# Kernel tuning notes

Measured on AMD Instinct MI355X. Metric: run time of the kernel, lower is better.

The kernel has to match this reference:

```python
import jax, jax.numpy as jnp
import numpy as np

B, H, K, HID = 64, 32, 4096, 7168
Q_LORA, KV_LORA = 1536, 512
NOPE, ROPE, VDIM = 128, 64, 128
HEAD_SIZE = NOPE + ROPE  # 192
EPS = 1e-6
SOFTMAX_SCALE = HEAD_SIZE ** -0.5  # mscale = 1 (no yarn)


def rmsnorm(x, w, eps=EPS):
    return x * jax.lax.rsqrt(jnp.mean(x * x, axis=-1, keepdims=True) + eps) * w


def interleave_rope(x, cos, sin):
    # x: [..., ROPE]; replicate torch view(d//2,2).transpose(2,3).reshape(d):
    # interleaved [r0,i0,r1,i1,...] -> [r0,r1,...,i0,i1,...], then rotate-half RoPE.
    shp = x.shape
    x = jnp.swapaxes(x.reshape(shp[:-1] + (ROPE // 2, 2)), -1, -2).reshape(shp)
    x1, x2 = x[..., : ROPE // 2], x[..., ROPE // 2:]
    # cos/sin: [B, ROPE//2] -> broadcast over head axis
    c = cos[:, None, :]
    s = sin[:, None, :]
    return jnp.concatenate([x1 * c - x2 * s, x2 * c + x1 * s], axis=-1)


def setup_inputs() -> dict:
    key = jax.random.key(0)
    ks = jax.random.split(key, 12)
    w = 0.02
    return {
        "hidden_states": jax.random.normal(ks[0], (B, HID), jnp.float32),
        "cos": jax.random.uniform(ks[1], (B, ROPE // 2), jnp.float32),
        "sin": jax.random.uniform(ks[2], (B, ROPE // 2), jnp.float32),
        "kv_cache": jax.random.normal(ks[3], (B, K, KV_LORA + ROPE), jnp.float32),
        "w_q_a": jax.random.normal(ks[4], (HID, Q_LORA), jnp.float32) * w,
        "q_a_ln_w": jnp.ones((Q_LORA,), jnp.float32),
        "w_q_b": jax.random.normal(ks[5], (Q_LORA, H * HEAD_SIZE), jnp.float32) * w,
        "w_kv_a": jax.random.normal(ks[6], (HID, KV_LORA + ROPE), jnp.float32) * w,
        "kv_a_ln_w": jnp.ones((KV_LORA,), jnp.float32),
        "w_uk_t": jax.random.normal(ks[7], (H, NOPE, KV_LORA), jnp.float32) * w,
        "w_uv": jax.random.normal(ks[8], (H, KV_LORA, VDIM), jnp.float32) * w,
        "w_o": jax.random.normal(ks[9], (H * VDIM, HID), jnp.float32) * w,
        "slots": jnp.full((B,), K - 1, jnp.int32),
        "seq_lens": jnp.full((B,), K, jnp.int32),
    }


def reference(hidden_states, cos, sin, kv_cache, w_q_a, q_a_ln_w, w_q_b,
              w_kv_a, kv_a_ln_w, w_uk_t, w_uv, w_o, slots, seq_lens):
    # --- Q low-rank path: q_a_proj -> RMSNorm -> q_b_proj ---
    q_c = rmsnorm(hidden_states @ w_q_a, q_a_ln_w)          # [B, Q_LORA]
    q = (q_c @ w_q_b).reshape(B, H, HEAD_SIZE)              # [B, H, 192]
    q_nope, q_pe = q[..., :NOPE], q[..., NOPE:]

    # --- K-up absorption: ql_nope = q_nope @ W_UK_T (per head) ---
    ql_nope = jnp.einsum("bhn,hnr->bhr", q_nope, w_uk_t)    # [B, H, KV_LORA]

    # --- compressed KV projection ---
    ckv = hidden_states @ w_kv_a                            # [B, KV_LORA+ROPE]
    kv_c, k_pe = ckv[:, :KV_LORA], ckv[:, KV_LORA:]
    kv_c = rmsnorm(kv_c, kv_a_ln_w)                         # [B, KV_LORA]
    k_pe = k_pe[:, None, :]                                 # [B, 1, ROPE]

    # --- interleaved RoPE on pe parts ---
    q_pe = interleave_rope(q_pe, cos, sin)                  # [B, H, ROPE]
    k_pe = interleave_rope(k_pe, cos, sin)[:, 0, :]         # [B, ROPE]

    # --- latent cache writeback ---
    latent_k = jnp.concatenate([kv_c, k_pe], axis=-1)       # [B, KV_LORA+ROPE]
    cache = kv_cache.at[jnp.arange(B), slots].set(latent_k)  # [B, K, 576]

    # --- MLA latent attention (decode) ---
    query = jnp.concatenate([ql_nope, q_pe], axis=-1)       # [B, H, 576]
    scores = jnp.einsum("bhd,bkd->bhk", query, cache) * SOFTMAX_SCALE
    valid = (jnp.arange(K)[None, :] < seq_lens[:, None])[:, None, :]  # [B,1,K]
    scores = jnp.where(valid, scores, jnp.finfo(scores.dtype).min)
    probs = jax.nn.softmax(scores, axis=-1)                 # [B, H, K]
    attn = jnp.einsum("bhk,bkr->bhr", probs, cache[..., :KV_LORA])  # [B,H,KV_LORA]

    # --- V-up absorption + output projection ---
    out = jnp.einsum("bhr,hrv->bhv", attn, w_uv)            # [B, H, VDIM]
    return out.reshape(B, H * VDIM) @ w_o                   # [B, HID]
```

## Files before the change

### kernel.cpp

```cpp
#include <hip/hip_runtime.h>
#include <stdint.h>

#define NB 64
#define NH 32
#define KCTX 4096
#define HID 7168
#define QLORA 1536
#define KVL 512
#define DTOT 576
#define NSPLIT 4
#define KSPAN 1024
#define NTILE 64
#define TK 16
#define SM_SCALE 0.07216878364870323f
#define NEGINF (-3.0e38f)

typedef __attribute__((ext_vector_type(4))) float f32x4;
typedef __attribute__((ext_vector_type(8))) __bf16 bf16x8;

#define LGKM_BARRIER() do{ asm volatile("s_waitcnt lgkmcnt(0)" ::: "memory"); __builtin_amdgcn_s_barrier(); } while(0)

static __device__ __forceinline__ void glds16(const void* g, void* s){
    __builtin_amdgcn_global_load_lds((const __attribute__((address_space(1))) void*)g,
                                     (__attribute__((address_space(3))) void*)s, 16, 0, 0);
}

static __device__ __forceinline__ unsigned short f2bf(float f){
    union{__bf16 h; unsigned short s;} x; x.h = (__bf16)f; return x.s;
}
static __device__ __forceinline__ float bf2f(unsigned short h){
    union{unsigned i;float f;}x; x.i=((unsigned)h)<<16; return x.f;
}
static __device__ __forceinline__ unsigned pack2(float a, float b){
    union{__bf16 h[2]; unsigned u;} x; x.h[0]=(__bf16)a; x.h[1]=(__bf16)b; return x.u;
}

template<int OUT_MODE>
static __device__ __forceinline__ void gemm_core_packed(
        const unsigned short* __restrict__ Ahi, const unsigned short* __restrict__ Alo,
        const float* __restrict__ Wm, float* __restrict__ P, int N, int ksteps,
        int bx, int by,
        unsigned short* Ah, unsigned short* Al, unsigned short* Bh, unsigned short* Bl)
{
    const int tid = threadIdx.x;
    const int w = tid>>6, l = tid&63, lm = l&15, lg = l>>4;
    const int n0 = bx*64;
    const int s  = by;
    const int mn = tid&63, ks = tid>>6;
    const int widx = ((mn>>4)*64 + ks*16 + (mn&15));

    f32x4 acc[4];
#pragma unroll
    for (int i=0;i<4;++i){ acc[i][0]=0.f; acc[i][1]=0.f; acc[i][2]=0.f; acc[i][3]=0.f; }

    uint4 ah4, al4; float wv[8];
    auto load_raw = [&](int t){
        const int k0 = (s*ksteps + t)*32;
        size_t gidx = (size_t)((k0>>3) + ks)*64 + mn;
        ah4 = *(const uint4*)(Ahi + gidx*8);
        al4 = *(const uint4*)(Alo + gidx*8);
        const float* wp = Wm + (size_t)(k0 + ks*8)*N + n0 + mn;
#pragma unroll
        for (int j=0;j<8;++j) wv[j] = wp[(size_t)j*N];
    };
    auto cvt_write = [&](int buf){
        unsigned short h8[8], l8[8];
#pragma unroll
        for (int j=0;j<8;++j){
            h8[j] = f2bf(wv[j]);
            l8[j] = f2bf(wv[j] - bf2f(h8[j]));
        }
        uint4 bh4, bl4;
        bh4.x=(unsigned)h8[0]|((unsigned)h8[1]<<16); bh4.y=(unsigned)h8[2]|((unsigned)h8[3]<<16);
        bh4.z=(unsigned)h8[4]|((unsigned)h8[5]<<16); bh4.w=(unsigned)h8[6]|((unsigned)h8[7]<<16);
        bl4.x=(unsigned)l8[0]|((unsigned)l8[1]<<16); bl4.y=(unsigned)l8[2]|((unsigned)l8[3]<<16);
        bl4.z=(unsigned)l8[4]|((unsigned)l8[5]<<16); bl4.w=(unsigned)l8[6]|((unsigned)l8[7]<<16);
        *(uint4*)(Ah + buf*2048 + widx*8) = ah4;
        *(uint4*)(Al + buf*2048 + widx*8) = al4;
        *(uint4*)(Bh + buf*2048 + widx*8) = bh4;
        *(uint4*)(Bl + buf*2048 + widx*8) = bl4;
    };

    load_raw(0);
    for (int t=0; t<ksteps; ++t){
        const int buf = t&1;
        cvt_write(buf);
        __syncthreads();
        if (t+1 < ksteps) load_raw(t+1);
        const int fa = buf*2048 + (w*64 + lg*16 + lm)*8;
        bf16x8 fah = *(const bf16x8*)(Ah + fa);
        bf16x8 fal = *(const bf16x8*)(Al + fa);
#pragma unroll
        for (int nt=0;nt<4;++nt){
            const int fb = buf*2048 + (nt*64 + lg*16 + lm)*8;
            bf16x8 fbh = *(const bf16x8*)(Bh + fb);
            bf16x8 fbl = *(const bf16x8*)(Bl + fb);
            acc[nt] = __builtin_amdgcn_mfma_f32_16x16x32_bf16(fah, fbh, acc[nt], 0,0,0);
            acc[nt] = __builtin_amdgcn_mfma_f32_16x16x32_bf16(fal, fbh, acc[nt], 0,0,0);
            acc[nt] = __builtin_amdgcn_mfma_f32_16x16x32_bf16(fah, fbl, acc[nt], 0,0,0);
        }
        __syncthreads();
    }
#pragma unroll
    for (int nt=0;nt<4;++nt){
        int n = n0 + nt*16 + lm;
#pragma unroll
        for (int r=0;r<4;++r){
            int m = w*16 + lg*4 + r;
            if (OUT_MODE == 0) P[((size_t)s*64 + m)*N + n] = acc[nt][r];
            else               unsafeAtomicAdd(&P[(size_t)m*N + n], acc[nt][r]);
        }
    }
}

static __device__ __forceinline__ void gemm_core_raw(
        const float* __restrict__ Araw, int KA,
        const float* __restrict__ Wm, float* __restrict__ P, int N, int ksteps,
        int bx, int by,
        unsigned short* Ah, unsigned short* Al, unsigned short* Bh, unsigned short* Bl)
{
    const int tid = threadIdx.x;
    const int w = tid>>6, l = tid&63, lm = l&15, lg = l>>4;
    const int n0 = bx*64;
    const int s  = by;
    const int mn = tid&63, ks = tid>>6;
    const int widx = ((mn>>4)*64 + ks*16 + (mn&15));

    f32x4 acc[4];
#pragma unroll
    for (int i=0;i<4;++i){ acc[i][0]=0.f; acc[i][1]=0.f; acc[i][2]=0.f; acc[i][3]=0.f; }

    float av[8], wv[8];
    auto load_raw = [&](int t){
        const int k0 = (s*ksteps + t)*32;
        const float* ap = Araw + (size_t)mn*KA + k0 + ks*8;
        *(float4*)(av)   = *(const float4*)(ap);
        *(float4*)(av+4) = *(const float4*)(ap+4);
        const float* wp = Wm + (size_t)(k0 + ks*8)*N + n0 + mn;
#pragma unroll
        for (int j=0;j<8;++j) wv[j] = wp[(size_t)j*N];
    };
    auto cvt_write = [&](int buf){
        unsigned short ha[8], la[8], hb[8], lb[8];
#pragma unroll
        for (int j=0;j<8;++j){
            ha[j] = f2bf(av[j]); la[j] = f2bf(av[j] - bf2f(ha[j]));
            hb[j] = f2bf(wv[j]); lb[j] = f2bf(wv[j] - bf2f(hb[j]));
        }
        uint4 ah4, al4, bh4, bl4;
        ah4.x=(unsigned)ha[0]|((unsigned)ha[1]<<16); ah4.y=(unsigned)ha[2]|((unsigned)ha[3]<<16);
        ah4.z=(unsigned)ha[4]|((unsigned)ha[5]<<16); ah4.w=(unsigned)ha[6]|((unsigned)ha[7]<<16);
        al4.x=(unsigned)la[0]|((unsigned)la[1]<<16); al4.y=(unsigned)la[2]|((unsigned)la[3]<<16);
        al4.z=(unsigned)la[4]|((unsigned)la[5]<<16); al4.w=(unsigned)la[6]|((unsigned)la[7]<<16);
        bh4.x=(unsigned)hb[0]|((unsigned)hb[1]<<16); bh4.y=(unsigned)hb[2]|((unsigned)hb[3]<<16);
        bh4.z=(unsigned)hb[4]|((unsigned)hb[5]<<16); bh4.w=(unsigned)hb[6]|((unsigned)hb[7]<<16);
        bl4.x=(unsigned)lb[0]|((unsigned)lb[1]<<16); bl4.y=(unsigned)lb[2]|((unsigned)lb[3]<<16);
        bl4.z=(unsigned)lb[4]|((unsigned)lb[5]<<16); bl4.w=(unsigned)lb[6]|((unsigned)lb[7]<<16);
        *(uint4*)(Ah + buf*2048 + widx*8) = ah4;
        *(uint4*)(Al + buf*2048 + widx*8) = al4;
        *(uint4*)(Bh + buf*2048 + widx*8) = bh4;
        *(uint4*)(Bl + buf*2048 + widx*8) = bl4;
    };

    load_raw(0);
    for (int t=0; t<ksteps; ++t){
        const int buf = t&1;
        cvt_write(buf);
        __syncthreads();
        if (t+1 < ksteps) load_raw(t+1);
        const int fa = buf*2048 + (w*64 + lg*16 + lm)*8;
        bf16x8 fah = *(const bf16x8*)(Ah + fa);
        bf16x8 fal = *(const bf16x8*)(Al + fa);
#pragma unroll
        for (int nt=0;nt<4;++nt){
            const int fb = buf*2048 + (nt*64 + lg*16 + lm)*8;
            bf16x8 fbh = *(const bf16x8*)(Bh + fb);
            bf16x8 fbl = *(const bf16x8*)(Bl + fb);
            acc[nt] = __builtin_amdgcn_mfma_f32_16x16x32_bf16(fah, fbh, acc[nt], 0,0,0);
            acc[nt] = __builtin_amdgcn_mfma_f32_16x16x32_bf16(fal, fbh, acc[nt], 0,0,0);
            acc[nt] = __builtin_amdgcn_mfma_f32_16x16x32_bf16(fah, fbl, acc[nt], 0,0,0);
        }
        __syncthreads();
    }
#pragma unroll
    for (int nt=0;nt<4;++nt){
        int n = n0 + nt*16 + lm;
#pragma unroll
        for (int r=0;r<4;++r){
            int m = w*16 + lg*4 + r;
            P[((size_t)s*64 + m)*N + n] = acc[nt][r];
        }
    }
}

__global__ __launch_bounds__(256) void gemm_mfma(
        const unsigned short* __restrict__ Ahi, const unsigned short* __restrict__ Alo,
        const float* __restrict__ Wm, float* __restrict__ P, int N, int ksteps)
{
    __shared__ unsigned short Ah[2*2048], Al[2*2048], Bh[2*2048], Bl[2*2048];
    gemm_core_packed<0>(Ahi, Alo, Wm, P, N, ksteps, blockIdx.x, blockIdx.y, Ah, Al, Bh, Bl);
}

__global__ __launch_bounds__(256) void gemm_atomic(
        const unsigned short* __restrict__ Ahi, const unsigned short* __restrict__ Alo,
        const float* __restrict__ Wm, float* __restrict__ Out, int N, int ksteps)
{
    __shared__ unsigned short Ah[2*2048], Al[2*2048], Bh[2*2048], Bl[2*2048];
    gemm_core_packed<1>(Ahi, Alo, Wm, Out, N, ksteps, blockIdx.x, blockIdx.y, Ah, Al, Bh, Bl);
}

__global__ __launch_bounds__(256) void gemm_dual_raw(
        const float* __restrict__ Araw, int KA,
        const float* __restrict__ W0, float* __restrict__ P0, int N0, int ks0, int nbx0, int nblk0,
        const float* __restrict__ W1, float* __restrict__ P1, int N1, int ks1, int nbx1)
{
    __shared__ unsigned short Ah[2*2048], Al[2*2048], Bh[2*2048], Bl[2*2048];
    int bid = blockIdx.x;
    if (bid < nblk0){
        gemm_core_raw(Araw, KA, W0, P0, N0, ks0, bid%nbx0, bid/nbx0, Ah, Al, Bh, Bl);
    } else {
        bid -= nblk0;
        gemm_core_raw(Araw, KA, W1, P1, N1, ks1, bid%nbx1, bid/nbx1, Ah, Al, Bh, Bl);
    }
}

static __device__ __forceinline__ void rms_core(const float* __restrict__ P,
        const float* __restrict__ w, unsigned short* __restrict__ Hi,
        unsigned short* __restrict__ Lo, int S, int b, float* red)
{
    const int t = threadIdx.x;
    float v[6]; float ss = 0.f;
#pragma unroll
    for (int j=0;j<6;++j){
        int n = j*256 + t;
        float s = 0.f;
        for (int sp=0; sp<S; ++sp) s += P[((size_t)sp*64+b)*1536 + n];
        v[j] = s; ss += s*s;
    }
#pragma unroll
    for (int off=32; off>=1; off>>=1) ss += __shfl_xor(ss, off, 64);
    if ((t&63)==0) red[t>>6] = ss;
    __syncthreads();
    float tot = red[0]+red[1]+red[2]+red[3];
    float rs = rsqrtf(tot/1536.f + 1e-6f);
#pragma unroll
    for (int j=0;j<6;++j){
        int n = j*256+t;
        float val = v[j]*rs*w[n];
        unsigned short hs = f2bf(val);
        unsigned short ls = f2bf(val - bf2f(hs));
        size_t ui = (size_t)(n>>3)*512 + b*8 + (n&7);
        Hi[ui] = hs; Lo[ui] = ls;
    }
}

static __device__ __forceinline__ void kvrope_core(const float* __restrict__ P,
        const float* __restrict__ w, const float* __restrict__ cosb, const float* __restrict__ sinb,
        float* __restrict__ latent, int S, int b, float* vals, float* red)
{
    const int t = threadIdx.x;
    float ss = 0.f;
    for (int j=0;j<3;++j){
        int n = j*256+t;
        if (n < 576){
            float s=0.f;
            for (int sp=0;sp<S;++sp) s += P[((size_t)sp*64+b)*576 + n];
            vals[n]=s;
            if (n<512) ss += s*s;
        }
    }
#pragma unroll
    for (int off=32; off>=1; off>>=1) ss += __shfl_xor(ss, off, 64);
    if ((t&63)==0) red[t>>6]=ss;
    __syncthreads();
    float tot = red[0]+red[1]+red[2]+red[3];
    float rs = rsqrtf(tot/512.f + 1e-6f);
    for (int j=0;j<3;++j){
        int n = j*256+t;
        if (n<576){
            float o;
            if (n < 512) o = vals[n]*rs*w[n];
            else if (n < 544){ int i=n-512; o = vals[512+2*i]*cosb[b*32+i] - vals[513+2*i]*sinb[b*32+i]; }
            else            { int i=n-544; o = vals[513+2*i]*cosb[b*32+i] + vals[512+2*i]*sinb[b*32+i]; }
            latent[(size_t)b*576 + n] = o;
        }
    }
}

__global__ __launch_bounds__(256) void norm_dual(
        const float* __restrict__ Pq, const float* __restrict__ qw,
        unsigned short* __restrict__ Hi, unsigned short* __restrict__ Lo, int Sq,
        const float* __restrict__ Pkv, const float* __restrict__ kvw,
        const float* __restrict__ cosb, const float* __restrict__ sinb,
        float* __restrict__ latent, int Skv)
{
    __shared__ float vals[576];
    __shared__ float red[4];
    if (blockIdx.x < 64) rms_core(Pq, qw, Hi, Lo, Sq, blockIdx.x, red);
    else                 kvrope_core(Pkv, kvw, cosb, sinb, latent, Skv, blockIdx.x-64, vals, red);
}

__global__ __launch_bounds__(256) void finish_q(const float* __restrict__ P,
        const float* __restrict__ cosb, const float* __restrict__ sinb,
        unsigned short* __restrict__ qh, unsigned short* __restrict__ ql,
        float* __restrict__ query, int S)
{
    int i = blockIdx.x*256 + threadIdx.x;
    int b = i / 6144, n = i - b*6144;
    float s = 0.f;
    for (int sp=0; sp<S; ++sp) s += P[((size_t)sp*64+b)*6144 + n];
    int h = n/192, nl = n - h*192;
    if (nl < 128){
        unsigned short hs = f2bf(s);
        unsigned short ls = f2bf(s - bf2f(hs));
        size_t ui = (size_t)h*8192 + (size_t)(nl>>3)*512 + b*8 + (nl&7);
        qh[ui]=hs; ql[ui]=ls;
    } else {
        int i2 = (nl-128)>>1;
        float other = __shfl_xor(s, 1);
        float c = cosb[b*32+i2], sn = sinb[b*32+i2];
        float* o = query + ((size_t)b*32+h)*576;
        if ((nl&1)==0) o[512+i2] = s*c - other*sn;
        else           o[544+i2] = s*c + other*sn;
    }
}

__global__ __launch_bounds__(256) void qlnope_mfma(const unsigned short* __restrict__ qh,
        const unsigned short* __restrict__ ql,
        const float* __restrict__ wukt, float* __restrict__ query)
{
    __shared__ unsigned short Bh[4096], Bl[4096];
    const int h = blockIdx.x, r0 = blockIdx.y*128;
    const int tid = threadIdx.x;
    const int w = tid>>6, l = tid&63, lm = l&15, lg = l>>4;
    f32x4 acc[8];
#pragma unroll
    for (int i=0;i<8;++i){ acc[i][0]=0.f; acc[i][1]=0.f; acc[i][2]=0.f; acc[i][3]=0.f; }

    for (int ck=0; ck<4; ++ck){
        const int k0 = ck*32;
        unsigned short hh[2][8], ll[2][8]; int wid0 = tid*2;
#pragma unroll
        for (int wi=0; wi<2; ++wi){
            int wid = wid0 + wi;
            int ntile = wid>>6, kg = (wid>>4)&3, nl = wid&15;
            int n = r0 + ntile*16 + nl;
            const float* wp = wukt + (size_t)h*65536 + (size_t)(k0+kg*8)*512 + n;
#pragma unroll
            for (int j=0;j<8;++j){
                float v = wp[(size_t)j*512];
                hh[wi][j] = f2bf(v);
                ll[wi][j] = f2bf(v - bf2f(hh[wi][j]));
            }
        }
        __syncthreads();
#pragma unroll
        for (int wi=0; wi<2; ++wi){
            int wid = wid0 + wi;
            uint4 uh, ul;
            uh.x=(unsigned)hh[wi][0]|((unsigned)hh[wi][1]<<16); uh.y=(unsigned)hh[wi][2]|((unsigned)hh[wi][3]<<16);
            uh.z=(unsigned)hh[wi][4]|((unsigned)hh[wi][5]<<16); uh.w=(unsigned)hh[wi][6]|((unsigned)hh[wi][7]<<16);
            ul.x=(unsigned)ll[wi][0]|((unsigned)ll[wi][1]<<16); ul.y=(unsigned)ll[wi][2]|((unsigned)ll[wi][3]<<16);
            ul.z=(unsigned)ll[wi][4]|((unsigned)ll[wi][5]<<16); ul.w=(unsigned)ll[wi][6]|((unsigned)ll[wi][7]<<16);
            *(uint4*)(Bh + wid*8) = uh;
            *(uint4*)(Bl + wid*8) = ul;
        }
        __syncthreads();
        size_t ai = (size_t)h*8192 + (size_t)(ck*4+lg)*512 + (size_t)(w*16+lm)*8;
        union{uint4 u; bf16x8 v;} fh, fl;
        fh.u = *(const uint4*)(qh + ai);
        fl.u = *(const uint4*)(ql + ai);
#pragma unroll
        for (int nt=0;nt<8;++nt){
            const int fb = (nt*64 + lg*16 + lm)*8;
            bf16x8 fbh = *(const bf16x8*)(Bh + fb);
            bf16x8 fbl = *(const bf16x8*)(Bl + fb);
            acc[nt] = __builtin_amdgcn_mfma_f32_16x16x32_bf16(fh.v, fbh, acc[nt], 0,0,0);
            acc[nt] = __builtin_amdgcn_mfma_f32_16x16x32_bf16(fl.v, fbh, acc[nt], 0,0,0);
            acc[nt] = __builtin_amdgcn_mfma_f32_16x16x32_bf16(fh.v, fbl, acc[nt], 0,0,0);
        }
        __syncthreads();
    }
#pragma unroll
    for (int nt=0;nt<8;++nt){
        int r = r0 + nt*16 + lm;
#pragma unroll
        for (int qq=0;qq<4;++qq){
            int bb = w*16 + lg*4 + qq;
            query[((size_t)bb*32 + h)*576 + r] = acc[nt][qq];
        }
    }
}

static __device__ __forceinline__ int vt_addr(int d, int key){
    return (d>>2)*64 + (((d&3)^((d>>3)&3))<<4) + key;
}

__global__ __launch_bounds__(512,1) void attn_mfma(const float* __restrict__ query,
        const float* __restrict__ kv, const float* __restrict__ latent,
        const int* __restrict__ slots, const int* __restrict__ seq_lens,
        float* __restrict__ Opart, float* __restrict__ Mpart, float* __restrict__ Lpart)
{
    __shared__ float Kf[3][16*576];
    __shared__ unsigned short Vt[8192];
    __shared__ float S_s[8][32][16];
    __shared__ unsigned short P_s[32][40];
    __shared__ float alpha_s[32];

    const int b = blockIdx.y, sp = blockIdx.x;
    const int tid = threadIdx.x;
    const int w = tid>>6, l = tid&63;
    const int lm = l&15, lg = l>>4;
    const int ht = w&1;
    const int dg = w>>1;
    const int cs = 2*w + (w>=1?1:0) + (w>=5?1:0);
    const int cnt = ((w&3)==0)?3:2;
    const int seqlen = seq_lens[b];
    const int slot = slots[b];
    const int k0 = sp*KSPAN;
    const int myh = tid>>4, s5 = tid&15;

    P_s[tid>>4][16 + (tid&15)] = 0;

    bf16x8 qf[2][3];
#pragma unroll
    for (int h2=0; h2<2; ++h2){
        const float* qrow = query + ((size_t)b*32 + h2*16 + lm)*576;
#pragma unroll
        for (int ss=0;ss<3;++ss){
            union{uint4 u; bf16x8 v;} cv;
            if (ss < cnt){
                int d0 = (cs+ss)*32 + lg*8;
                float4 a = *(const float4*)(qrow + d0);
                float4 c = *(const float4*)(qrow + d0 + 4);
                cv.u.x=pack2(a.x,a.y); cv.u.y=pack2(a.z,a.w);
                cv.u.z=pack2(c.x,c.y); cv.u.w=pack2(c.z,c.w);
            } else {
                cv.u.x=0; cv.u.y=0; cv.u.z=0; cv.u.w=0;
            }
            qf[h2][ss]=cv.v;
        }
    }

    auto issue_tile = [&](int tt, int buf){
        const int gkb = k0 + tt*TK;
#pragma unroll
        for (int i=0;i<5;++i){
            int s = i*8 + w;
            if (s < 36){
                int B = s*1024 + l*16;
                int r = B / 2304;
                int gs = (B - r*2304) >> 4;
                int g  = gs ^ (r&7);
                int gk = gkb + r; if (gk > KCTX-1) gk = KCTX-1;
                const float* src = (gk==slot) ? (latent + (size_t)b*576 + g*4)
                                              : (kv + ((size_t)b*KCTX + gk)*576 + g*4);
                glds16(src, ((char*)&Kf[buf][0]) + B);
            }
        }
    };

    f32x4 oacc[8];
#pragma unroll
    for (int i=0;i<8;++i){ oacc[i][0]=0.f; oacc[i][1]=0.f; oacc[i][2]=0.f; oacc[i][3]=0.f; }
    float m_run = NEGINF, l_run = 0.f;

    issue_tile(0, 0);
    issue_tile(1, 1);
    if (w < 4) { asm volatile("s_waitcnt vmcnt(5)" ::: "memory"); }
    else       { asm volatile("s_waitcnt vmcnt(4)" ::: "memory"); }
    __builtin_amdgcn_s_barrier();

    int cur = 0;
    for (int tt=0; tt<NTILE; ++tt){
        if (tt+2 < NTILE){
            int ib = cur+2; if (ib>=3) ib-=3;
            issue_tile(tt+2, ib);
        }

        {
            const int kg = tid&1;
            const int dq = (tid>>1)&127;
            const int rep = tid>>8;
            float4 rv[4];
#pragma unroll
            for (int i=0;i<4;++i){
                int r = kg*8 + rep*4 + i;
                rv[i] = *(const float4*)(&Kf[cur][r*576 + ((dq ^ (r&7))<<2)]);
            }
#pragma unroll
            for (int j=0;j<4;++j){
                uint2 o;
                o.x = pack2(((const float*)&rv[0])[j], ((const float*)&rv[1])[j]);
                o.y = pack2(((const float*)&rv[2])[j], ((const float*)&rv[3])[j]);
                *(uint2*)(Vt + vt_addr(dq*4+j, kg*8) + rep*4) = o;
            }
        }
        {
            f32x4 s0, s1;
            s0[0]=0.f; s0[1]=0.f; s0[2]=0.f; s0[3]=0.f;
            s1[0]=0.f; s1[1]=0.f; s1[2]=0.f; s1[3]=0.f;
            const float* kb = &Kf[cur][lm*576];
            const int sw = lm&7;
            __builtin_amdgcn_s_setprio(1);
#pragma unroll
            for (int ss=0;ss<3;++ss){
                if (ss < cnt){
                    int g = (cs+ss)*8 + lg*2;
                    float4 fa = *(const float4*)(kb + ((g ^ sw)<<2));
                    float4 fb = *(const float4*)(kb + (((g+1) ^ sw)<<2));
                    union{uint4 u; bf16x8 v;} cv;
                    cv.u.x = pack2(fa.x, fa.y); cv.u.y = pack2(fa.z, fa.w);
                    cv.u.z = pack2(fb.x, fb.y); cv.u.w = pack2(fb.z, fb.w);
                    s0 = __builtin_amdgcn_mfma_f32_16x16x32_bf16(qf[0][ss], cv.v, s0, 0,0,0);
                    s1 = __builtin_amdgcn_mfma_f32_16x16x32_bf16(qf[1][ss], cv.v, s1, 0,0,0);
                }
            }
            __builtin_amdgcn_s_setprio(0);
#pragma unroll
            for (int r=0;r<4;++r){
                S_s[w][(lg<<2)+r][lm]      = s0[r];
                S_s[w][16+(lg<<2)+r][lm]   = s1[r];
            }
        }
        LGKM_BARRIER();

        {
            const int kbase = k0 + tt*TK;
            float v = 0.f;
#pragma unroll
            for (int i=0;i<8;++i) v += S_s[i][myh][s5];
            v *= SM_SCALE;
            float sc = (kbase + s5 < seqlen) ? v : NEGINF;
            float tmax = sc;
            tmax = fmaxf(tmax, __shfl_xor(tmax,1));
            tmax = fmaxf(tmax, __shfl_xor(tmax,2));
            tmax = fmaxf(tmax, __shfl_xor(tmax,4));
            tmax = fmaxf(tmax, __shfl_xor(tmax,8));
            float mnew = fmaxf(m_run, tmax);
            float al = __expf(m_run - mnew);
            float pv = (sc > 0.5f*NEGINF) ? __expf(sc-mnew) : 0.f;
            P_s[myh][s5] = f2bf(pv);
            float ps = pv;
            ps += __shfl_xor(ps,1); ps += __shfl_xor(ps,2);
            ps += __shfl_xor(ps,4); ps += __shfl_xor(ps,8);
            l_run = l_run*al + ps;
            m_run = mnew;
            if (s5==0) alpha_s[myh] = al;
        }
        LGKM_BARRIER();

        {
            float al4[4];
#pragma unroll
            for (int r=0;r<4;++r) al4[r] = alpha_s[ht*16 + (lg<<2) + r];
            bf16x8 pa = *(const bf16x8*)(&P_s[ht*16+lm][lg*8]);
            __builtin_amdgcn_s_setprio(1);
#pragma unroll
            for (int nt=0;nt<8;++nt){
                f32x4 o = oacc[nt];
                o[0]*=al4[0]; o[1]*=al4[1]; o[2]*=al4[2]; o[3]*=al4[3];
                int r = dg*128 + nt*16 + lm;
                bf16x8 bv = *(const bf16x8*)(Vt + vt_addr(r, (lg&1)*8));
                oacc[nt] = __builtin_amdgcn_mfma_f32_16x16x32_bf16(pa, bv, o, 0,0,0);
            }
            __builtin_amdgcn_s_setprio(0);
        }
        if (tt+2 < NTILE){
            if (w < 4) { asm volatile("s_waitcnt vmcnt(5)" ::: "memory"); }
            else       { asm volatile("s_waitcnt vmcnt(4)" ::: "memory"); }
            __builtin_amdgcn_s_barrier();
        } else if (tt+1 < NTILE){
            asm volatile("s_waitcnt vmcnt(0)" ::: "memory");
            __builtin_amdgcn_s_barrier();
        }
        cur = cur+1; if (cur>=3) cur-=3;
    }

    const int obase = (b*NSPLIT+sp)*32;
#pragma unroll
    for (int nt=0;nt<8;++nt){
        int r = dg*128 + nt*16 + lm;
#pragma unroll
        for (int qq=0;qq<4;++qq){
            int h = ht*16 + (lg<<2) + qq;
            Opart[((size_t)(obase+h))*512 + r] = oacc[nt][qq];
        }
    }
    if (s5==0){ Mpart[obase+myh]=m_run; Lpart[obase+myh]=l_run; }
}

__global__ __launch_bounds__(256) void av_uv_merge(const float* __restrict__ Opart,
        const float* __restrict__ Mpart, const float* __restrict__ Lpart,
        const float* __restrict__ wuv,
        unsigned short* __restrict__ Hi, unsigned short* __restrict__ Lo)
{
    __shared__ unsigned short Bh[4096], Bl[4096];
    __shared__ unsigned short Ah[512], Al[512];
    __shared__ float lwn[16][4];
    const int h = blockIdx.x, bg = blockIdx.y;
    const int tid = threadIdx.x;
    const int w = tid>>6, l = tid&63, lm = l&15, lg = l>>4;

    if (tid < 16){
        int b = bg*16 + tid;
        float m0 = Mpart[(b*NSPLIT+0)*32+h], m1 = Mpart[(b*NSPLIT+1)*32+h];
        float m2 = Mpart[(b*NSPLIT+2)*32+h], m3 = Mpart[(b*NSPLIT+3)*32+h];
        float M = fmaxf(fmaxf(m0,m1),fmaxf(m2,m3));
        float w0 = __expf(m0-M), w1 = __expf(m1-M), w2 = __expf(m2-M), w3 = __expf(m3-M);
        float L = w0*Lpart[(b*NSPLIT+0)*32+h] + w1*Lpart[(b*NSPLIT+1)*32+h]
                + w2*Lpart[(b*NSPLIT+2)*32+h] + w3*Lpart[(b*NSPLIT+3)*32+h];
        float inv = 1.f/L;
        lwn[tid][0]=w0*inv; lwn[tid][1]=w1*inv; lwn[tid][2]=w2*inv; lwn[tid][3]=w3*inv;
    }
    __syncthreads();

    f32x4 acc[2];
#pragma unroll
    for (int i=0;i<2;++i){ acc[i][0]=0.f; acc[i][1]=0.f; acc[i][2]=0.f; acc[i][3]=0.f; }

    for (int ck=0; ck<16; ++ck){
        const int k0 = ck*32;
        unsigned short hh[2][8], ll[2][8]; int wid0 = tid*2;
#pragma unroll
        for (int wi=0; wi<2; ++wi){
            int wid = wid0 + wi;
            int ntile = wid>>6, kg = (wid>>4)&3, nl = wid&15;
            int n = ntile*16 + nl;
            const float* wp = wuv + (size_t)h*65536 + (size_t)(k0+kg*8)*128 + n;
#pragma unroll
            for (int j=0;j<8;++j){
                float v = wp[(size_t)j*128];
                hh[wi][j] = f2bf(v);
                ll[wi][j] = f2bf(v - bf2f(hh[wi][j]));
            }
        }
        float av[2];
#pragma unroll
        for (int e=0;e<2;++e){
            int id = tid*2+e;
            int row = id>>5, k = id&31;
            int bb = bg*16 + row;
            const float* op = Opart + (((size_t)bb*NSPLIT)*32 + h)*512 + k0 + k;
            av[e] = lwn[row][0]*op[0] + lwn[row][1]*op[16384]
                  + lwn[row][2]*op[32768] + lwn[row][3]*op[49152];
        }
        __syncthreads();
#pragma unroll
        for (int wi=0; wi<2; ++wi){
            int wid = wid0 + wi;
            uint4 uh, ul;
            uh.x=(unsigned)hh[wi][0]|((unsigned)hh[wi][1]<<16); uh.y=(unsigned)hh[wi][2]|((unsigned)hh[wi][3]<<16);
            uh.z=(unsigned)hh[wi][4]|((unsigned)hh[wi][5]<<16); uh.w=(unsigned)hh[wi][6]|((unsigned)hh[wi][7]<<16);
            ul.x=(unsigned)ll[wi][0]|((unsigned)ll[wi][1]<<16); ul.y=(unsigned)ll[wi][2]|((unsigned)ll[wi][3]<<16);
            ul.z=(unsigned)ll[wi][4]|((unsigned)ll[wi][5]<<16); ul.w=(unsigned)ll[wi][6]|((unsigned)ll[wi][7]<<16);
            *(uint4*)(Bh + wid*8) = uh;
            *(uint4*)(Bl + wid*8) = ul;
        }
#pragma unroll
        for (int e=0;e<2;++e){
            int id = tid*2+e;
            int row = id>>5, k = id&31;
            unsigned short hs = f2bf(av[e]);
            unsigned short ls = f2bf(av[e] - bf2f(hs));
            int ai = ((k>>3)*16 + row)*8 + (k&7);
            Ah[ai] = hs; Al[ai] = ls;
        }
        __syncthreads();
        const int fa = (lg*16 + lm)*8;
        bf16x8 fah = *(const bf16x8*)(Ah + fa);
        bf16x8 fal = *(const bf16x8*)(Al + fa);
#pragma unroll
        for (int i=0;i<2;++i){
            int nt = w*2 + i;
            const int fb = (nt*64 + lg*16 + lm)*8;
            bf16x8 fbh = *(const bf16x8*)(Bh + fb);
            bf16x8 fbl = *(const bf16x8*)(Bl + fb);
            acc[i] = __builtin_amdgcn_mfma_f32_16x16x32_bf16(fah, fbh, acc[i], 0,0,0);
            acc[i] = __builtin_amdgcn_mfma_f32_16x16x32_bf16(fal, fbh, acc[i], 0,0,0);
            acc[i] = __builtin_amdgcn_mfma_f32_16x16x32_bf16(fah, fbl, acc[i], 0,0,0);
        }
        __syncthreads();
    }
#pragma unroll
    for (int i=0;i<2;++i){
        int nt = w*2 + i;
#pragma unroll
        for (int qq=0;qq<4;++qq){
            float val = acc[i][qq];
            int bb = bg*16 + lg*4 + qq;
            int k = h*128 + nt*16 + lm;
            unsigned short hv = f2bf(val);
            unsigned short lv = f2bf(val - bf2f(hv));
            size_t ui = (size_t)(k>>3)*512 + bb*8 + (k&7);
            Hi[ui] = hv; Lo[ui] = lv;
        }
    }
}

extern "C" void kernel_launch(void* const* d_in, const int* in_sizes, int n_in,
                              void* d_out, int out_size, void* d_ws, size_t ws_size,
                              hipStream_t stream)
{
    const float* hidden = (const float*)d_in[0];
    const float* cosb   = (const float*)d_in[1];
    const float* sinb   = (const float*)d_in[2];
    const float* kv     = (const float*)d_in[3];
    const float* w_q_a  = (const float*)d_in[4];
    const float* q_ln   = (const float*)d_in[5];
    const float* w_q_b  = (const float*)d_in[6];
    const float* w_kv_a = (const float*)d_in[7];
    const float* kv_ln  = (const float*)d_in[8];
    const float* w_uk_t = (const float*)d_in[9];
    const float* w_uv   = (const float*)d_in[10];
    const float* w_o    = (const float*)d_in[11];
    const int* slots    = (const int*)d_in[12];
    const int* seqlens  = (const int*)d_in[13];
    float* out = (float*)d_out;

    float* W = (float*)d_ws;
    float* P0     = W;
    float* P1     = W + 4194304;
    float* query  = W + 6291456;
    float* latent = W + 7471104;
    float* Mp     = W + 7507968;
    float* Lp     = W + 7516160;
    unsigned short* pkq_h  = (unsigned short*)(W + 7524352);
    unsigned short* pkq_l  = (unsigned short*)(W + 7655424);
    unsigned short* pkqc_h = (unsigned short*)(W + 7786496);
    unsigned short* pkqc_l = (unsigned short*)(W + 7835648);
    unsigned short* pkao_h = (unsigned short*)(W + 7884800);
    unsigned short* pkao_l = (unsigned short*)(W + 8015872);

    hipMemsetAsync(out, 0, (size_t)NB*HID*sizeof(float), stream);

    hipLaunchKernelGGL(gemm_dual_raw, dim3(672+252), dim3(256), 0, stream,
                       hidden, HID, w_q_a, P0, 1536, 8, 24, 672, w_kv_a, P1, 576, 8, 9);
    hipLaunchKernelGGL(norm_dual, dim3(128), dim3(256), 0, stream,
                       P0, q_ln, pkqc_h, pkqc_l, 28, P1, kv_ln, cosb, sinb, latent, 28);
    hipLaunchKernelGGL(gemm_mfma, dim3(96,6), dim3(256), 0, stream, pkqc_h, pkqc_l, w_q_b, P0, 6144, 8);
    hipLaunchKernelGGL(finish_q, dim3(1536), dim3(256), 0, stream, P0, cosb, sinb, pkq_h, pkq_l, query, 6);
    hipLaunchKernelGGL(qlnope_mfma, dim3(32,4), dim3(256), 0, stream, pkq_h, pkq_l, w_uk_t, query);
    hipLaunchKernelGGL(attn_mfma, dim3(NSPLIT,64), dim3(512), 0, stream,
                       query, kv, latent, slots, seqlens, P0, Mp, Lp);
    hipLaunchKernelGGL(av_uv_merge, dim3(32,4), dim3(256), 0, stream, P0, Mp, Lp, w_uv, pkao_h, pkao_l);
    hipLaunchKernelGGL(gemm_atomic, dim3(112,8), dim3(256), 0, stream, pkao_h, pkao_l, w_o, out, 7168, 16);
}
```

Baseline: 328.3 us.

## Triple-buffer packed GEMM with async global-to-LDS loads and in-loop bf16 split

Reworks the packed-A GEMM core (used by gemm_mfma and gemm_atomic) to use a three-stage LDS ring filled directly by global_load_lds, issuing tiles two steps ahead. Raw fp32 weights are kept in LDS, and each wave splits them into bf16 hi/lo just before the MFMAs, replacing the old register staging plus convert-and-store pass. This removes one barrier per step and lets memory latency overlap with compute. In exchange, every wave repeats the weight conversion, LDS use grows, and the strided fp32 LDS reads may hit bank conflicts.

```diff
diff --git a/kernel.cpp b/kernel.cpp
--- a/kernel.cpp
+++ b/kernel.cpp
@@ -40,66 +40,76 @@
         const unsigned short* __restrict__ Ahi, const unsigned short* __restrict__ Alo,
         const float* __restrict__ Wm, float* __restrict__ P, int N, int ksteps,
         int bx, int by,
-        unsigned short* Ah, unsigned short* Al, unsigned short* Bh, unsigned short* Bl)
+        unsigned short* Ah3, unsigned short* Al3, float* Wf3)
 {
     const int tid = threadIdx.x;
     const int w = tid>>6, l = tid&63, lm = l&15, lg = l>>4;
     const int n0 = bx*64;
     const int s  = by;
-    const int mn = tid&63, ks = tid>>6;
-    const int widx = ((mn>>4)*64 + ks*16 + (mn&15));
 
     f32x4 acc[4];
 #pragma unroll
     for (int i=0;i<4;++i){ acc[i][0]=0.f; acc[i][1]=0.f; acc[i][2]=0.f; acc[i][3]=0.f; }
 
-    uint4 ah4, al4; float wv[8];
-    auto load_raw = [&](int t){
-        const int k0 = (s*ksteps + t)*32;
-        size_t gidx = (size_t)((k0>>3) + ks)*64 + mn;
-        ah4 = *(const uint4*)(Ahi + gidx*8);
-        al4 = *(const uint4*)(Alo + gidx*8);
-        const float* wp = Wm + (size_t)(k0 + ks*8)*N + n0 + mn;
-#pragma unroll
-        for (int j=0;j<8;++j) wv[j] = wp[(size_t)j*N];
+    auto issue_tile = [&](int t, int buf){
+        const int k0g = (s*ksteps + t)*32;
+        size_t ga = (size_t)((k0g>>3) + w)*64 + l;
+        glds16(Ahi + ga*8, Ah3 + buf*2048 + tid*8);
+        glds16(Alo + ga*8, Al3 + buf*2048 + tid*8);
+#pragma unroll
+        for (int i=0;i<2;++i){
+            int c = tid + i*256;
+            int r = c>>4, c4 = (c&15)<<2;
+            glds16(Wm + (size_t)(k0g+r)*N + n0 + c4, Wf3 + buf*2048 + c*4);
+        }
     };
-    auto cvt_write = [&](int buf){
-        unsigned short h8[8], l8[8];
-#pragma unroll
-        for (int j=0;j<8;++j){
-            h8[j] = f2bf(wv[j]);
-            l8[j] = f2bf(wv[j] - bf2f(h8[j]));
-        }
-        uint4 bh4, bl4;
-        bh4.x=(unsigned)h8[0]|((unsigned)h8[1]<<16); bh4.y=(unsigned)h8[2]|((unsigned)h8[3]<<16);
-        bh4.z=(unsigned)h8[4]|((unsigned)h8[5]<<16); bh4.w=(unsigned)h8[6]|((unsigned)h8[7]<<16);
-        bl4.x=(unsigned)l8[0]|((unsigned)l8[1]<<16); bl4.y=(unsigned)l8[2]|((unsigned)l8[3]<<16);
-        bl4.z=(unsigned)l8[4]|((unsigned)l8[5]<<16); bl4.w=(unsigned)l8[6]|((unsigned)l8[7]<<16);
-        *(uint4*)(Ah + buf*2048 + widx*8) = ah4;
-        *(uint4*)(Al + buf*2048 + widx*8) = al4;
-        *(uint4*)(Bh + buf*2048 + widx*8) = bh4;
-        *(uint4*)(Bl + buf*2048 + widx*8) = bl4;
-    };
-
-    load_raw(0);
+
+    issue_tile(0, 0);
+    if (ksteps > 1) issue_tile(1, 1);
+    asm volatile("s_waitcnt vmcnt(4)" ::: "memory");
+    __builtin_amdgcn_s_barrier();
+
+    int cur = 0;
     for (int t=0; t<ksteps; ++t){
-        const int buf = t&1;
-        cvt_write(buf);
-        __syncthreads();
-        if (t+1 < ksteps) load_raw(t+1);
-        const int fa = buf*2048 + (w*64 + lg*16 + lm)*8;
-        bf16x8 fah = *(const bf16x8*)(Ah + fa);
-        bf16x8 fal = *(const bf16x8*)(Al + fa);
+        if (t+2 < ksteps){
+            int ib = cur+2; if (ib>=3) ib-=3;
+            issue_tile(t+2, ib);
+        }
+        const unsigned short* Ahb = Ah3 + cur*2048;
+        const unsigned short* Alb = Al3 + cur*2048;
+        const float* Wb = Wf3 + cur*2048;
+        const int fa = (lg*64 + w*16 + lm)*8;
+        bf16x8 fah = *(const bf16x8*)(Ahb + fa);
+        bf16x8 fal = *(const bf16x8*)(Alb + fa);
 #pragma unroll
         for (int nt=0;nt<4;++nt){
-            const int fb = buf*2048 + (nt*64 + lg*16 + lm)*8;
-            bf16x8 fbh = *(const bf16x8*)(Bh + fb);
-            bf16x8 fbl = *(const bf16x8*)(Bl + fb);
-            acc[nt] = __builtin_amdgcn_mfma_f32_16x16x32_bf16(fah, fbh, acc[nt], 0,0,0);
-            acc[nt] = __builtin_amdgcn_mfma_f32_16x16x32_bf16(fal, fbh, acc[nt], 0,0,0);
-            acc[nt] = __builtin_amdgcn_mfma_f32_16x16x32_bf16(fah, fbl, acc[nt], 0,0,0);
-        }
-        __syncthreads();
+            const float* wb = Wb + lg*512 + nt*16 + lm;
+            float wv[8];
+#pragma unroll
+            for (int j=0;j<8;++j) wv[j] = wb[(size_t)j*64];
+            unsigned short hb8[8], lb8[8];
+#pragma unroll
+            for (int j=0;j<8;++j){
+                hb8[j] = f2bf(wv[j]);
+                lb8[j] = f2bf(wv[j] - bf2f(hb8[j]));
+            }
+            union{uint4 u; bf16x8 v;} fbh, fbl;
+            fbh.u.x=(unsigned)hb8[0]|((unsigned)hb8[1]<<16); fbh.u.y=(unsigned)hb8[2]|((unsigned)hb8[3]<<16);
+            fbh.u.z=(unsigned)hb8[4]|((unsigned)hb8[5]<<16); fbh.u.w=(unsigned)hb8[6]|((unsigned)hb8[7]<<16);
+            fbl.u.x=(unsigned)lb8[0]|((unsigned)lb8[1]<<16); fbl.u.y=(unsigned)lb8[2]|((unsigned)lb8[3]<<16);
+            fbl.u.z=(unsigned)lb8[4]|((unsigned)lb8[5]<<16); fbl.u.w=(unsigned)lb8[6]|((unsigned)lb8[7]<<16);
+            acc[nt] = __builtin_amdgcn_mfma_f32_16x16x32_bf16(fah, fbh.v, acc[nt], 0,0,0);
+            acc[nt] = __builtin_amdgcn_mfma_f32_16x16x32_bf16(fal, fbh.v, acc[nt], 0,0,0);
+            acc[nt] = __builtin_amdgcn_mfma_f32_16x16x32_bf16(fah, fbl.v, acc[nt], 0,0,0);
+        }
+        if (t+2 < ksteps){
+            asm volatile("s_waitcnt vmcnt(4)" ::: "memory");
+            __builtin_amdgcn_s_barrier();
+        } else if (t+1 < ksteps){
+            asm volatile("s_waitcnt vmcnt(0)" ::: "memory");
+            __builtin_amdgcn_s_barrier();
+        }
+        cur = cur+1; if (cur>=3) cur-=3;
     }
 #pragma unroll
     for (int nt=0;nt<4;++nt){
@@ -197,16 +207,18 @@
         const unsigned short* __restrict__ Ahi, const unsigned short* __restrict__ Alo,
         const float* __restrict__ Wm, float* __restrict__ P, int N, int ksteps)
 {
-    __shared__ unsigned short Ah[2*2048], Al[2*2048], Bh[2*2048], Bl[2*2048];
-    gemm_core_packed<0>(Ahi, Alo, Wm, P, N, ksteps, blockIdx.x, blockIdx.y, Ah, Al, Bh, Bl);
+    __shared__ unsigned short Ah3[3*2048], Al3[3*2048];
+    __shared__ float Wf3[3*2048];
+    gemm_core_packed<0>(Ahi, Alo, Wm, P, N, ksteps, blockIdx.x, blockIdx.y, Ah3, Al3, Wf3);
 }
 
 __global__ __launch_bounds__(256) void gemm_atomic(
         const unsigned short* __restrict__ Ahi, const unsigned short* __restrict__ Alo,
         const float* __restrict__ Wm, float* __restrict__ Out, int N, int ksteps)
 {
-    __shared__ unsigned short Ah[2*2048], Al[2*2048], Bh[2*2048], Bl[2*2048];
-    gemm_core_packed<1>(Ahi, Alo, Wm, Out, N, ksteps, blockIdx.x, blockIdx.y, Ah, Al, Bh, Bl);
+    __shared__ unsigned short Ah3[3*2048], Al3[3*2048];
+    __shared__ float Wf3[3*2048];
+    gemm_core_packed<1>(Ahi, Alo, Wm, Out, N, ksteps, blockIdx.x, blockIdx.y, Ah3, Al3, Wf3);
 }
 
 __global__ __launch_bounds__(256) void gemm_dual_raw(
```

After: 348.8 us. 1.06x slower.
